# Kernel optimization log

Hardware: AMD Instinct MI355X
Metric: run time of the kernel (lower is better)

The kernel has to match this reference:

```python
import jax, jax.numpy as jnp
from jax import lax
import numpy as np

B, T, H, L = 4096, 7, 512, 256
D = 2 * H  # bidirectional LSTM feature dim


def _lstm(x, wih, whh, bih, bhh, reverse):
    # x: [B, T, L]; torch gate order i, f, g, o
    b, hdim = x.shape[0], whh.shape[0]
    xs = jnp.swapaxes(x, 0, 1)  # [T, B, L]
    bias = bih + bhh

    def step(carry, xt):
        h, c = carry
        gates = xt @ wih + h @ whh + bias
        i, f, g, o = jnp.split(gates, 4, axis=-1)
        c = jax.nn.sigmoid(f) * c + jax.nn.sigmoid(i) * jnp.tanh(g)
        h = jax.nn.sigmoid(o) * jnp.tanh(c)
        return (h, c), h

    h0 = jnp.zeros((b, hdim), x.dtype)
    _, hs = lax.scan(step, (h0, h0), xs, reverse=reverse)
    return jnp.swapaxes(hs, 0, 1)  # [B, T, H]


def _att(enc, dec):
    # Sequential attention: keys/values start as enc and grow with each decoder output.
    keys = enc  # [B, T, D]
    outs = []
    for i in range(dec.shape[1]):  # fixed small T=7, Python loop is static
        q = dec[:, i, :]                                  # [B, D]
        scores = jnp.einsum('bd,btd->bt', q, keys)        # dot over features
        a = jax.nn.softmax(scores, axis=1)
        ctx = jnp.einsum('bt,btd->bd', a, keys)
        out = ctx + q
        outs.append(out)
        keys = jnp.concatenate([keys, out[:, None, :]], axis=1)
    return jnp.stack(outs, axis=1)  # [B, T, D]


def _deconv(x, w, b):
    # torch ConvTranspose2d (stride 1, pad 0) == full conv with flipped, in/out-swapped kernel
    kh, kw = w.shape[2], w.shape[3]
    w2 = jnp.transpose(w[:, :, ::-1, ::-1], (1, 0, 2, 3))  # [out, in, kh, kw]
    y = lax.conv_general_dilated(x, w2, (1, 1), ((kh - 1, kh - 1), (kw - 1, kw - 1)),
                                 dimension_numbers=('NCHW', 'OIHW', 'NCHW'))
    return y + b[None, :, None, None]


def setup_inputs() -> dict:
    key = jax.random.key(0)
    ks = jax.random.split(key, 12)
    p = lambda k, shape: jax.random.normal(k, shape, jnp.float32) * 0.02
    return {
        'lstm_enc': jax.random.normal(ks[0], (B, T, D), jnp.float32),
        'gaussian_noise': jax.random.normal(ks[1], (B, L), jnp.float32),
        'embedrep_w': p(ks[2], (L, L * T)), 'embedrep_b': jnp.zeros((L * T,), jnp.float32),
        'wih_f': p(ks[3], (L, 4 * H)), 'whh_f': p(ks[4], (H, 4 * H)),
        'bih_f': jnp.zeros((4 * H,), jnp.float32), 'bhh_f': jnp.zeros((4 * H,), jnp.float32),
        'wih_b': p(ks[5], (L, 4 * H)), 'whh_b': p(ks[6], (H, 4 * H)),
        'bih_b': jnp.zeros((4 * H,), jnp.float32), 'bhh_b': jnp.zeros((4 * H,), jnp.float32),
        'emb_w': p(ks[7], (D, 1024)), 'emb_b': jnp.zeros((1024,), jnp.float32),
        'dc3_w': p(ks[8], (64, 32, 1, 3)), 'dc3_b': jnp.zeros((32,), jnp.float32),
        'dc1_w': p(ks[9], (32, 16, 1, 5)), 'dc1_b': jnp.zeros((16,), jnp.float32),
        'dc2_w': p(ks[10], (16, 1, 3, 3)), 'dc2_b': jnp.zeros((1,), jnp.float32),
        'infer': 0,
    }


def reference(lstm_enc, gaussian_noise, embedrep_w, embedrep_b,
              wih_f, whh_f, bih_f, bhh_f, wih_b, whh_b, bih_b, bhh_b,
              emb_w, emb_b, dc3_w, dc3_b, dc1_w, dc1_b, dc2_w, dc2_b, infer):
    b = lstm_enc.shape[0]
    g1 = jax.nn.soft_sign(gaussian_noise @ embedrep_w + embedrep_b)   # [B, L*T]
    rep = g1.reshape(b, T, L)                                          # [B, 7, L]
    hf = _lstm(rep, wih_f, whh_f, bih_f, bhh_f, False)
    hb = _lstm(rep, wih_b, whh_b, bih_b, bhh_b, True)
    lstm1 = jnp.concatenate([hf, hb], axis=-1)                         # [B, 7, 2H]
    att_out = _att(lstm_enc, lstm1)                                    # [B, 7, 2H]
    emb = att_out @ emb_w + emb_b                                      # [B, 7, 1024]
    up = jax.nn.soft_sign(emb).reshape(b * T, 64, 1, 16)
    x = jax.nn.leaky_relu(_deconv(up, dc3_w, dc3_b))                   # [B*7, 32, 1, 18]
    x = jax.nn.leaky_relu(_deconv(x, dc1_w, dc1_b))                    # [B*7, 16, 1, 22]
    x = jax.nn.leaky_relu(_deconv(x, dc2_w, dc2_b))                    # [B*7, 1, 3, 24]
    x = jax.nn.softmax(x, axis=2)                                      # softmax over H dim (=3)
    out = x.reshape(b, T, 1, 3, 24)[:, :, -1, :, :]                    # [B, 7, 3, 24]
    return out
```

## Files before the change

### kernel.cpp

```cpp
#include <hip/hip_runtime.h>
#include <stdint.h>


typedef __attribute__((ext_vector_type(4))) float f32x4;
typedef __attribute__((ext_vector_type(8))) short bf16x8;
typedef __attribute__((ext_vector_type(4))) unsigned short us4;

__device__ __forceinline__ unsigned short f2b(float f) {
  union { float f; unsigned u; } x; x.f = f;
  unsigned r = x.u + 0x7FFFu + ((x.u >> 16) & 1u);
  return (unsigned short)(r >> 16);
}
__device__ __forceinline__ float b2f(unsigned short s) {
  union { unsigned u; float f; } x; x.u = ((unsigned)s) << 16; return x.f;
}
__device__ __forceinline__ float sigmoidf(float x) {
  return 1.f / (1.f + __expf(-x));
}
__device__ __forceinline__ float fast_tanh(float x) {
  x = fminf(15.f, fmaxf(-15.f, x));
  float e = __expf(2.f * x);
  return (e - 1.f) / (e + 1.f);
}

__device__ __forceinline__ void gl_lds16(const void* g, void* l) {
  auto gp = reinterpret_cast<const __attribute__((address_space(1))) unsigned int*>(
      reinterpret_cast<uintptr_t>(g));
  auto lp = reinterpret_cast<__attribute__((address_space(3))) unsigned int*>(
      reinterpret_cast<uintptr_t>(l));
  __builtin_amdgcn_global_load_lds(gp, lp, 16, 0, 0);
}


__device__ __forceinline__ void stage256x32(const unsigned short* src, int ld,
                                            unsigned short* hbase, int tid) {
  const int row_in = tid >> 2;
  const int gidx = tid & 3;
#pragma unroll
  for (int r = 0; r < 4; ++r) {
    int row = r * 64 + row_in;
    int gsrc = gidx ^ ((row >> 1) & 3);
    gl_lds16(src + (size_t)row * ld + gsrc * 8, hbase + r * 2048 + (tid >> 6) * 512);
  }
}

__device__ __forceinline__ void stage128x32(const unsigned short* src, int ld,
                                            unsigned short* hbase, int tid) {
  const int row_in = tid >> 2;
  const int gidx = tid & 3;
#pragma unroll
  for (int r = 0; r < 2; ++r) {
    int row = r * 64 + row_in;
    int gsrc = gidx ^ ((row >> 1) & 3);
    gl_lds16(src + (size_t)row * ld + gsrc * 8, hbase + r * 2048 + (tid >> 6) * 512);
  }
}

__device__ __forceinline__ bf16x8 lds_fragH(const unsigned short* hbase, int row, int lq) {
  return *(const bf16x8*)(hbase + row * 32 + (lq ^ (((row >> 1) & 3) << 3)));
}

__device__ __forceinline__ void tile_w128(const unsigned short* Ab, const unsigned short* Bb,
                                          int wm, int wn, int lane, f32x4 (&acc)[8][4]) {
  const int lr = lane & 15, lq = (lane >> 4) * 8;
  bf16x8 b[4];
#pragma unroll
  for (int n = 0; n < 4; ++n) b[n] = lds_fragH(Bb, wn * 64 + n * 16 + lr, lq);
  bf16x8 a[8];
#pragma unroll
  for (int i = 0; i < 8; ++i) a[i] = lds_fragH(Ab, wm * 128 + i * 16 + lr, lq);
  __builtin_amdgcn_s_setprio(1);
#pragma unroll
  for (int i = 0; i < 8; ++i)
#pragma unroll
    for (int n = 0; n < 4; ++n)
      acc[i][n] = __builtin_amdgcn_mfma_f32_16x16x32_bf16(a[i], b[n], acc[i][n], 0, 0, 0);
  __builtin_amdgcn_s_setprio(0);
}

#define DBUF_SYNC()                                   \
  asm volatile("s_waitcnt vmcnt(0)" ::: "memory");    \
  __builtin_amdgcn_s_barrier();                       \
  __builtin_amdgcn_sched_barrier(0);

__device__ __forceinline__ void stage128x64(const unsigned short* src, int ld,
                                            unsigned short* lds, int wv, int lane) {
#pragma unroll
  for (int r = 0; r < 4; ++r) {
    int row = r * 32 + wv * 8 + (lane >> 3);
    gl_lds16(src + (size_t)row * ld + (lane & 7) * 8, lds + (r * 32 + wv * 8) * 64);
  }
}
__device__ __forceinline__ void mfma_tile(const unsigned short* As, const unsigned short* Bs,
                                          int wm, int wn, int lane, f32x4 acc[4][4]) {
#pragma unroll
  for (int kk = 0; kk < 2; ++kk) {
    int ko = kk * 32 + (lane >> 4) * 8;
    bf16x8 a[4], b[4];
#pragma unroll
    for (int i = 0; i < 4; ++i)
      a[i] = *(const bf16x8*)(As + (size_t)(wm * 64 + i * 16 + (lane & 15)) * 64 + ko);
#pragma unroll
    for (int i = 0; i < 4; ++i)
      b[i] = *(const bf16x8*)(Bs + (size_t)(wn * 64 + i * 16 + (lane & 15)) * 64 + ko);
#pragma unroll
    for (int mi = 0; mi < 4; ++mi)
#pragma unroll
      for (int ni = 0; ni < 4; ++ni)
        acc[mi][ni] = __builtin_amdgcn_mfma_f32_16x16x32_bf16(a[mi], b[ni], acc[mi][ni], 0, 0, 0);
  }
}

__global__ __launch_bounds__(256) void pack_kernel(
    const float* __restrict__ noise, const float* __restrict__ erep_w,
    const float* __restrict__ emb_w,
    const float* __restrict__ wih_f, const float* __restrict__ whh_f,
    const float* __restrict__ bih_f, const float* __restrict__ bhh_f,
    const float* __restrict__ wih_b, const float* __restrict__ whh_b,
    const float* __restrict__ bih_b, const float* __restrict__ bhh_b,
    unsigned short* __restrict__ noiseb, unsigned short* __restrict__ erepT,
    unsigned short* __restrict__ embT, unsigned short* __restrict__ lstmW,
    float* __restrict__ lstmB) {
  const int N0 = 4096 * 256;
  const int N1 = 1792 * 256;
  const int N2 = 1024 * 1024;
  const int N3 = 2 * 2048 * 768;
  const int N4 = 2 * 2048;
  const int total = N0 + N1 + N2 + N3 + N4;
  for (int i = blockIdx.x * 256 + threadIdx.x; i < total; i += gridDim.x * 256) {
    int x = i;
    if (x < N0) { noiseb[x] = f2b(noise[x]); continue; }
    x -= N0;
    if (x < N1) { int n = x >> 8, k = x & 255; erepT[x] = f2b(erep_w[k * 1792 + n]); continue; }
    x -= N1;
    if (x < N2) {
      int n = x >> 10, k = x & 1023;
      int o = (n & 63) * 16 + (n >> 6);
      embT[x] = f2b(emb_w[k * 1024 + o]);
      continue;
    }
    x -= N2;
    if (x < N3) {
      int dir = x / (2048 * 768);
      int r = x - dir * (2048 * 768);
      int npk = r / 768, k = r - (r / 768) * 768;
      int blk = npk >> 6, g = (npk >> 4) & 3, u = npk & 15;
      int o = g * 512 + blk * 16 + u;
      const float* wih = dir ? wih_b : wih_f;
      const float* whh = dir ? whh_b : whh_f;
      float v = (k < 256) ? wih[k * 2048 + o] : whh[(k - 256) * 2048 + o];
      lstmW[x] = f2b(v);
      continue;
    }
    x -= N3;
    {
      int dir = x >> 11, npk = x & 2047;
      int blk = npk >> 6, g = (npk >> 4) & 3, u = npk & 15;
      int o = g * 512 + blk * 16 + u;
      lstmB[x] = dir ? (bih_b[o] + bhh_b[o]) : (bih_f[o] + bhh_f[o]);
    }
  }
}

__global__ __launch_bounds__(256) void gemm_rep_kernel(
    const unsigned short* __restrict__ A, const unsigned short* __restrict__ Bt,
    const float* __restrict__ bias, unsigned short* __restrict__ rep_t) {
  __shared__ unsigned short As[128 * 64];
  __shared__ unsigned short Bs[128 * 64];
  const int lane = threadIdx.x & 63, wv = threadIdx.x >> 6;
  const int wm = wv >> 1, wn = wv & 1;
  const int m0 = blockIdx.y * 128, n0 = blockIdx.x * 128;
  f32x4 acc[4][4];
#pragma unroll
  for (int i = 0; i < 4; ++i)
#pragma unroll
    for (int j = 0; j < 4; ++j) acc[i][j] = (f32x4){0.f, 0.f, 0.f, 0.f};
  for (int k0 = 0; k0 < 256; k0 += 64) {
    stage128x64(A + (size_t)m0 * 256 + k0, 256, As, wv, lane);
    stage128x64(Bt + (size_t)n0 * 256 + k0, 256, Bs, wv, lane);
    __syncthreads();
    mfma_tile(As, Bs, wm, wn, lane, acc);
    __syncthreads();
  }
#pragma unroll
  for (int ni = 0; ni < 4; ++ni) {
    int n = n0 + wn * 64 + ni * 16 + (lane & 15);
    float bv = bias[n];
    int t = n >> 8, l = n & 255;
#pragma unroll
    for (int mi = 0; mi < 4; ++mi)
#pragma unroll
      for (int r = 0; r < 4; ++r) {
        int m = m0 + wm * 64 + mi * 16 + (lane >> 4) * 4 + r;
        float v = acc[mi][ni][r] + bv;
        v = v / (1.f + fabsf(v));
        rep_t[((size_t)t * 4096 + m) * 256 + l] = f2b(v);
      }
  }
}

__global__ __launch_bounds__(256, 2) void lstm_step_kernel(
    const unsigned short* __restrict__ rep_t, const unsigned short* __restrict__ Wp,
    const float* __restrict__ biasP, unsigned short* __restrict__ hbuf,
    unsigned short* __restrict__ cbuf, unsigned short* __restrict__ lstm1, int step) {
  __shared__ unsigned short Ar[2][8192];
  __shared__ unsigned short Br[2][4096];
  const int tid = threadIdx.x, lane = tid & 63, wv = tid >> 6;
  const int wm = wv >> 1, wn = wv & 1;
  const int swz = (blockIdx.x & 7) * 64 + (blockIdx.x >> 3);
  const int dir = swz >> 8;
  const int rem = swz & 255;
  const int by = rem >> 4, bx = rem & 15;
  const int m0 = by * 256, n0 = bx * 128;
  const int t_proc = dir ? (6 - step) : step;
  const unsigned short* W = Wp + (size_t)dir * 2048 * 768;
  const unsigned short* hin = hbuf + ((size_t)(step & 1) * 2 + dir) * (4096 * 512);
  unsigned short* hout = hbuf + ((size_t)((step + 1) & 1) * 2 + dir) * (4096 * 512);
  unsigned short* cp = cbuf + (size_t)dir * (4096 * 512);
  const unsigned short* xsrc = rep_t + (size_t)t_proc * 4096 * 256;

  f32x4 acc[8][4];
#pragma unroll
  for (int i = 0; i < 8; ++i)
#pragma unroll
    for (int j = 0; j < 4; ++j) acc[i][j] = (f32x4){0.f, 0.f, 0.f, 0.f};

  auto asrc = [&](int tt) {
    return tt < 8 ? xsrc + (size_t)m0 * 256 + tt * 32
                  : hin + (size_t)m0 * 512 + (tt - 8) * 32;
  };
  auto ald = [&](int tt) { return tt < 8 ? 256 : 512; };

  stage256x32(asrc(0), ald(0), Ar[0], tid);
  stage128x32(W + (size_t)n0 * 768 + 0 * 32, 768, Br[0], tid);
  DBUF_SYNC()

#pragma unroll
  for (int t = 0; t < 24; ++t) {
    if (t + 1 < 24) {
      stage256x32(asrc(t + 1), ald(t + 1), Ar[(t + 1) & 1], tid);
      stage128x32(W + (size_t)n0 * 768 + (t + 1) * 32, 768, Br[(t + 1) & 1], tid);
    }
    tile_w128(Ar[t & 1], Br[t & 1], wm, wn, lane, acc);
    if (t + 1 < 24) { DBUF_SYNC() }
  }

  const int u = lane & 15;
  const int blk = (n0 + wn * 64) >> 6;
  const int j = blk * 16 + u;
  const float bz0 = biasP[dir * 2048 + blk * 64 + 0 * 16 + u];
  const float bz1 = biasP[dir * 2048 + blk * 64 + 1 * 16 + u];
  const float bz2 = biasP[dir * 2048 + blk * 64 + 2 * 16 + u];
  const float bz3 = biasP[dir * 2048 + blk * 64 + 3 * 16 + u];
#pragma unroll
  for (int mi = 0; mi < 8; ++mi)
#pragma unroll
    for (int r = 0; r < 4; ++r) {
      int row = m0 + wm * 128 + mi * 16 + (lane >> 4) * 4 + r;
      float gi = acc[mi][0][r] + bz0;
      float gf = acc[mi][1][r] + bz1;
      float gg = acc[mi][2][r] + bz2;
      float go = acc[mi][3][r] + bz3;
      size_t ci = (size_t)row * 512 + j;
      float c = sigmoidf(gf) * b2f(cp[ci]) + sigmoidf(gi) * fast_tanh(gg);
      cp[ci] = f2b(c);
      float h = sigmoidf(go) * fast_tanh(c);
      unsigned short hb = f2b(h);
      hout[ci] = hb;
      lstm1[((size_t)row * 7 + t_proc) * 1024 + dir * 512 + j] = hb;
    }
}

__global__ __launch_bounds__(256) void att_fused3_kernel(
    const float* __restrict__ enc, const unsigned short* __restrict__ lstm1,
    unsigned short* __restrict__ att) {
  __shared__ unsigned short Qs[7 * 1032];
  __shared__ unsigned short Es[7 * 1032];
  __shared__ float P[8 * 256];
  __shared__ float sG[98];
  __shared__ float sC[7][14];
  __shared__ float sA[16];
  const int tid = threadIdx.x, lane = tid & 63, wv = tid >> 6;
  const int b = blockIdx.x;
  const float* Eb = enc + (size_t)b * 7168;
  const unsigned short* Qb = lstm1 + (size_t)b * 7168;

  if (tid < 98) ((float*)sC)[tid] = 0.f;

  const f32x4* Eb4 = (const f32x4*)Eb;
  const int d0 = tid * 4;
#pragma unroll
  for (int r = 0; r < 7; ++r) {
    f32x4 v = Eb4[r * 256 + tid];
    us4 hi;
#pragma unroll
    for (int e = 0; e < 4; ++e) hi[e] = f2b(v[e]);
    *(us4*)&Es[r * 1032 + d0] = hi;
    *(us4*)&Qs[r * 1032 + d0] = *(const us4*)(Qb + r * 1024 + d0);
  }
  asm volatile("s_waitcnt lgkmcnt(0)" ::: "memory");
  __builtin_amdgcn_sched_barrier(0);

  {
    const int rr = lane & 15;
    const int rowc = rr % 7;
    const int kbase = wv * 256 + (lane >> 4) * 8;
    f32x4 g1 = {0.f, 0.f, 0.f, 0.f}, g2 = {0.f, 0.f, 0.f, 0.f};
#pragma unroll
    for (int s = 0; s < 8; ++s) {
      const int k0 = kbase + s * 32;
      bf16x8 aq = *(const bf16x8*)&Qs[rowc * 1032 + k0];
      bf16x8 be = *(const bf16x8*)&Es[rowc * 1032 + k0];
      g1 = __builtin_amdgcn_mfma_f32_16x16x32_bf16(aq, be, g1, 0, 0, 0);
      g2 = __builtin_amdgcn_mfma_f32_16x16x32_bf16(aq, aq, g2, 0, 0, 0);
    }
    *(f32x4*)&P[((wv * 2 + 0) * 64 + lane) * 4] = g1;
    *(f32x4*)&P[((wv * 2 + 1) * 64 + lane) * 4] = g2;
  }
  __syncthreads();

  if (tid < 98) {
    int i = tid / 14, v = tid - i * 14;
    int col = v < 7 ? v : v - 7;
    int tile = v < 7 ? 0 : 1;
    int ln = ((i >> 2) << 4) | col;
    int rg = i & 3;
    float s = 0.f;
#pragma unroll
    for (int w = 0; w < 4; ++w) s += P[((w * 2 + tile) * 64 + ln) * 4 + rg];
    sG[i * 14 + v] = s;
  }
  __syncthreads();
  if (wv == 0) {
    for (int i = 0; i < 7; ++i) {
      const int nt = 7 + i;
      float s = -1e30f;
      if (lane < 7) {
        s = sG[i * 14 + lane];
      } else if (lane < nt) {
        int jj = lane - 7;
        float a2 = 0.f;
#pragma unroll
        for (int v = 0; v < 14; ++v) a2 += sC[jj][v] * sG[i * 14 + v];
        s = a2;
      }
      float mx = s;
#pragma unroll
      for (int off = 8; off >= 1; off >>= 1) mx = fmaxf(mx, __shfl_xor(mx, off, 16));
      float e = (lane < nt) ? __expf(s - mx) : 0.f;
      float sum = e;
#pragma unroll
      for (int off = 8; off >= 1; off >>= 1) sum += __shfl_xor(sum, off, 16);
      float aw = e / sum;
      if (lane < 16) sA[lane] = aw;
      if (lane < 14) {
        float c = (lane < 7) ? sA[lane] : 0.f;
        for (int jj = 0; jj < i; ++jj) c += sA[7 + jj] * sC[jj][lane];
        if (lane == 7 + i) c += 1.f;
        sC[i][lane] = c;
      }
    }
  }
  __syncthreads();

  {
    float acc[7][4];
#pragma unroll
    for (int i = 0; i < 7; ++i)
#pragma unroll
      for (int e = 0; e < 4; ++e) acc[i][e] = 0.f;
#pragma unroll
    for (int t = 0; t < 7; ++t) {
      us4 ev = *(const us4*)&Es[t * 1032 + d0];
      float evf[4];
#pragma unroll
      for (int e = 0; e < 4; ++e) evf[e] = b2f(ev[e]);
#pragma unroll
      for (int i = 0; i < 7; ++i) {
        float c = sC[i][t];
#pragma unroll
        for (int e = 0; e < 4; ++e) acc[i][e] += c * evf[e];
      }
    }
#pragma unroll
    for (int m = 0; m < 7; ++m) {
      us4 qv = *(const us4*)&Qs[m * 1032 + d0];
      float qf[4];
#pragma unroll
      for (int e = 0; e < 4; ++e) qf[e] = b2f(qv[e]);
#pragma unroll
      for (int i = m; i < 7; ++i) {
        float c = sC[i][7 + m];
#pragma unroll
        for (int e = 0; e < 4; ++e) acc[i][e] += c * qf[e];
      }
    }
    unsigned short* Ab = att + (size_t)b * 7168;
#pragma unroll
    for (int i = 0; i < 7; ++i) {
      us4 r;
#pragma unroll
      for (int e = 0; e < 4; ++e) r[e] = f2b(acc[i][e]);
      *(us4*)(Ab + i * 1024 + d0) = r;
    }
  }
}

__global__ __launch_bounds__(256, 2) void gemm_emb_kernel(
    const unsigned short* __restrict__ A, const unsigned short* __restrict__ Bt,
    const float* __restrict__ bias, unsigned short* __restrict__ up_t) {
  __shared__ unsigned short Ar[2][8192];
  __shared__ unsigned short Br[2][4096];
  const int tid = threadIdx.x, lane = tid & 63, wv = tid >> 6;
  const int wm = wv >> 1, wn = wv & 1;
  const int swz = (blockIdx.x & 7) * 112 + (blockIdx.x >> 3);
  const int by = swz >> 3, bx = swz & 7;
  const int m0 = by * 256, n0 = bx * 128;

  f32x4 acc[8][4];
#pragma unroll
  for (int i = 0; i < 8; ++i)
#pragma unroll
    for (int j = 0; j < 4; ++j) acc[i][j] = (f32x4){0.f, 0.f, 0.f, 0.f};

  const unsigned short* Abase = A + (size_t)m0 * 1024;
  const unsigned short* Bbase = Bt + (size_t)n0 * 1024;

  stage256x32(Abase + 0 * 32, 1024, Ar[0], tid);
  stage128x32(Bbase + 0 * 32, 1024, Br[0], tid);
  DBUF_SYNC()

#pragma unroll
  for (int t = 0; t < 32; ++t) {
    if (t + 1 < 32) {
      stage256x32(Abase + (t + 1) * 32, 1024, Ar[(t + 1) & 1], tid);
      stage128x32(Bbase + (t + 1) * 32, 1024, Br[(t + 1) & 1], tid);
    }
    tile_w128(Ar[t & 1], Br[t & 1], wm, wn, lane, acc);
    if (t + 1 < 32) { DBUF_SYNC() }
  }

#pragma unroll
  for (int ni = 0; ni < 4; ++ni) {
    int np = n0 + wn * 64 + ni * 16 + (lane & 15);
    int o = (np & 63) * 16 + (np >> 6);
    float bv = bias[o];
#pragma unroll
    for (int mi = 0; mi < 8; ++mi)
#pragma unroll
      for (int r = 0; r < 4; ++r) {
        int m = m0 + wm * 128 + mi * 16 + (lane >> 4) * 4 + r;
        float v = acc[mi][ni][r] + bv;
        v = v / (1.f + fabsf(v));
        up_t[(size_t)m * 1024 + np] = f2b(v);
      }
  }
}

__global__ __launch_bounds__(256) void dc_fused_kernel(
    const unsigned short* __restrict__ up_t,
    const float* __restrict__ w3, const float* __restrict__ b3,
    const float* __restrict__ w1, const float* __restrict__ b1,
    const float* __restrict__ w2, const float* __restrict__ b2,
    float* __restrict__ out) {
  __shared__ unsigned short y1L[576 * 40];
  __shared__ unsigned short y2L[704 * 24];
  const int tid = threadIdx.x, lane = tid & 63, wv = tid >> 6;
  const int g0 = blockIdx.x * 32;
  const int kq = (lane >> 4) * 8;
  const int oc = lane & 15;

  {
    bf16x8 bf[2][6];
#pragma unroll
    for (int nt = 0; nt < 2; ++nt)
#pragma unroll
      for (int kk = 0; kk < 6; ++kk) {
        bf16x8 v;
#pragma unroll
        for (int t = 0; t < 8; ++t) {
          int k = kk * 32 + kq + t;
          int jj = k >> 6, ic = k & 63;
          v[t] = (short)f2b(w3[((size_t)ic * 32 + nt * 16 + oc) * 3 + jj]);
        }
        bf[nt][kk] = v;
      }
    const float bia0 = b3[oc], bia1 = b3[16 + oc];
    for (int c = wv; c < 36; c += 4) {
      int m = c * 16 + (lane & 15);
      int imgl = m / 18, ow = m - imgl * 18;
      const unsigned short* arow = up_t + (size_t)(g0 + imgl) * 1024;
      f32x4 acc0 = {0.f, 0.f, 0.f, 0.f}, acc1 = {0.f, 0.f, 0.f, 0.f};
#pragma unroll
      for (int kk = 0; kk < 6; ++kk) {
        int jj = kk >> 1;
        int ic0 = (kk & 1) * 32 + kq;
        int iw = ow - jj;
        bf16x8 a = {0, 0, 0, 0, 0, 0, 0, 0};
        if ((unsigned)iw < 16u) a = *(const bf16x8*)(arow + iw * 64 + ic0);
        acc0 = __builtin_amdgcn_mfma_f32_16x16x32_bf16(a, bf[0][kk], acc0, 0, 0, 0);
        acc1 = __builtin_amdgcn_mfma_f32_16x16x32_bf16(a, bf[1][kk], acc1, 0, 0, 0);
      }
#pragma unroll
      for (int r = 0; r < 4; ++r) {
        int mm = c * 16 + (lane >> 4) * 4 + r;
        float v0 = acc0[r] + bia0; v0 = v0 > 0.f ? v0 : 0.01f * v0;
        float v1 = acc1[r] + bia1; v1 = v1 > 0.f ? v1 : 0.01f * v1;
        y1L[mm * 40 + oc] = f2b(v0);
        y1L[mm * 40 + 16 + oc] = f2b(v1);
      }
    }
  }
  __syncthreads();

  {
    bf16x8 bf[5];
#pragma unroll
    for (int kk = 0; kk < 5; ++kk) {
      bf16x8 v;
#pragma unroll
      for (int t = 0; t < 8; ++t) {
        int ic = kq + t;
        v[t] = (short)f2b(w1[((size_t)ic * 16 + oc) * 5 + kk]);
      }
      bf[kk] = v;
    }
    const float bia = b1[oc];
    for (int c = wv; c < 44; c += 4) {
      int m = c * 16 + (lane & 15);
      int imgl = m / 22, ow = m - imgl * 22;
      const unsigned short* abase = y1L + imgl * (18 * 40);
      f32x4 acc = {0.f, 0.f, 0.f, 0.f};
#pragma unroll
      for (int kk = 0; kk < 5; ++kk) {
        int iw = ow - kk;
        bf16x8 a = {0, 0, 0, 0, 0, 0, 0, 0};
        if ((unsigned)iw < 18u) a = *(const bf16x8*)(abase + iw * 40 + kq);
        acc = __builtin_amdgcn_mfma_f32_16x16x32_bf16(a, bf[kk], acc, 0, 0, 0);
      }
#pragma unroll
      for (int r = 0; r < 4; ++r) {
        int mm = c * 16 + (lane >> 4) * 4 + r;
        float v = acc[r] + bia;
        v = v > 0.f ? v : 0.01f * v;
        y2L[mm * 24 + oc] = f2b(v);
      }
    }
  }
  __syncthreads();

  for (int ii = tid; ii < 768; ii += 256) {
    int imgl = ii / 24, ow = ii - imgl * 24;
    float lg0 = b2[0], lg1 = b2[0], lg2 = b2[0];
#pragma unroll
    for (int jj = 0; jj < 3; ++jj) {
      int iw = ow - jj;
      if ((unsigned)iw >= 22u) continue;
      const unsigned short* row = y2L + (imgl * 22 + iw) * 24;
      bf16x8 v0 = *(const bf16x8*)(row);
      bf16x8 v1 = *(const bf16x8*)(row + 8);
      float x[16];
#pragma unroll
      for (int ic = 0; ic < 8; ++ic) {
        x[ic] = b2f((unsigned short)v0[ic]);
        x[8 + ic] = b2f((unsigned short)v1[ic]);
      }
#pragma unroll
      for (int ic = 0; ic < 16; ++ic) {
        lg0 += x[ic] * w2[ic * 9 + 0 * 3 + jj];
        lg1 += x[ic] * w2[ic * 9 + 1 * 3 + jj];
        lg2 += x[ic] * w2[ic * 9 + 2 * 3 + jj];
      }
    }
    lg0 = lg0 > 0.f ? lg0 : 0.01f * lg0;
    lg1 = lg1 > 0.f ? lg1 : 0.01f * lg1;
    lg2 = lg2 > 0.f ? lg2 : 0.01f * lg2;
    float mx = fmaxf(lg0, fmaxf(lg1, lg2));
    float e0 = __expf(lg0 - mx), e1 = __expf(lg1 - mx), e2 = __expf(lg2 - mx);
    float inv = 1.f / (e0 + e1 + e2);
    size_t ob = (size_t)(g0 + imgl) * 72 + ow;
    out[ob] = e0 * inv;
    out[ob + 24] = e1 * inv;
    out[ob + 48] = e2 * inv;
  }
}

extern "C" void kernel_launch(void* const* d_in, const int* in_sizes, int n_in,
                              void* d_out, int out_size, void* d_ws, size_t ws_size,
                              hipStream_t stream) {
  (void)in_sizes; (void)n_in; (void)out_size; (void)ws_size;
  const float* enc    = (const float*)d_in[0];
  const float* noise  = (const float*)d_in[1];
  const float* erep_w = (const float*)d_in[2];
  const float* erep_b = (const float*)d_in[3];
  const float* wih_f  = (const float*)d_in[4];
  const float* whh_f  = (const float*)d_in[5];
  const float* bih_f  = (const float*)d_in[6];
  const float* bhh_f  = (const float*)d_in[7];
  const float* wih_b  = (const float*)d_in[8];
  const float* whh_b  = (const float*)d_in[9];
  const float* bih_b  = (const float*)d_in[10];
  const float* bhh_b  = (const float*)d_in[11];
  const float* emb_w  = (const float*)d_in[12];
  const float* emb_b  = (const float*)d_in[13];
  const float* dc3w   = (const float*)d_in[14];
  const float* dc3b   = (const float*)d_in[15];
  const float* dc1w   = (const float*)d_in[16];
  const float* dc1b   = (const float*)d_in[17];
  const float* dc2w   = (const float*)d_in[18];
  const float* dc2b   = (const float*)d_in[19];
  float* out = (float*)d_out;

  char* p = (char*)d_ws;
  auto carve = [&p](size_t bytes) {
    char* r = p;
    p += (bytes + 255) & ~(size_t)255;
    return r;
  };
  unsigned short* rep_t  = (unsigned short*)carve(7ull * 4096 * 256 * 2);
  unsigned short* lstmW  = (unsigned short*)carve(2ull * 2048 * 768 * 2);
  float*          lstmB  = (float*)carve(2ull * 2048 * 4);
  unsigned short* noiseb = (unsigned short*)carve(4096ull * 256 * 2);
  unsigned short* erepT  = (unsigned short*)carve(1792ull * 256 * 2);
  unsigned short* embT   = (unsigned short*)carve(1024ull * 1024 * 2);
  unsigned short* hbuf   = (unsigned short*)carve(4ull * 4096 * 512 * 2);
  unsigned short* cbuf   = (unsigned short*)carve(2ull * 4096 * 512 * 2);
  unsigned short* lstm1  = (unsigned short*)carve(4096ull * 7 * 1024 * 2);
  unsigned short* att    = (unsigned short*)carve(28672ull * 1024 * 2);
  unsigned short* up_t   = (unsigned short*)carve(28672ull * 1024 * 2);

  hipMemsetAsync(hbuf, 0, 2ull * 4096 * 512 * 2, stream);
  hipMemsetAsync(cbuf, 0, 2ull * 4096 * 512 * 2, stream);

  pack_kernel<<<2048, 256, 0, stream>>>(noise, erep_w, emb_w, wih_f, whh_f, bih_f, bhh_f,
                                        wih_b, whh_b, bih_b, bhh_b,
                                        noiseb, erepT, embT, lstmW, lstmB);
  gemm_rep_kernel<<<dim3(14, 32), 256, 0, stream>>>(noiseb, erepT, erep_b, rep_t);
  for (int s = 0; s < 7; ++s)
    lstm_step_kernel<<<512, 256, 0, stream>>>(rep_t, lstmW, lstmB, hbuf, cbuf, lstm1, s);
  att_fused3_kernel<<<4096, 256, 0, stream>>>(enc, lstm1, att);
  gemm_emb_kernel<<<896, 256, 0, stream>>>(att, embT, emb_b, up_t);
  dc_fused_kernel<<<896, 256, 0, stream>>>(up_t, dc3w, dc3b, dc1w, dc1b, dc2w, dc2b, out);
}
```

Measured before the change: 497.1 us.

## Halve LSTM step tile to 128 rows with 2-wave blocks; vectorize pack kernel

Each LSTM step block now covers a 128x128 output tile with 128 threads (2 waves), and twice as many blocks are launched. The goal is more blocks per step so the GPU's CUs are better filled. Separately, the weight-pack kernel now converts four elements per thread and writes them as one vector store. The smaller tile gives up some reuse of the weight tile across rows and adds more staging traffic per output.

```diff
diff --git a/kernel.cpp b/kernel.cpp
--- a/kernel.cpp
+++ b/kernel.cpp
@@ -53,6 +53,18 @@
     int row = r * 64 + row_in;
     int gsrc = gidx ^ ((row >> 1) & 3);
     gl_lds16(src + (size_t)row * ld + gsrc * 8, hbase + r * 2048 + (tid >> 6) * 512);
+  }
+}
+
+__device__ __forceinline__ void stage128x32_t128(const unsigned short* src, int ld,
+                                                 unsigned short* hbase, int tid) {
+  const int row_in = tid >> 2;
+  const int gidx = tid & 3;
+#pragma unroll
+  for (int r = 0; r < 4; ++r) {
+    int row = r * 32 + row_in;
+    int gsrc = gidx ^ ((row >> 1) & 3);
+    gl_lds16(src + (size_t)row * ld + gsrc * 8, hbase + r * 1024 + (tid >> 6) * 512);
   }
 }
 
@@ -121,43 +133,71 @@
     unsigned short* __restrict__ noiseb, unsigned short* __restrict__ erepT,
     unsigned short* __restrict__ embT, unsigned short* __restrict__ lstmW,
     float* __restrict__ lstmB) {
-  const int N0 = 4096 * 256;
-  const int N1 = 1792 * 256;
-  const int N2 = 1024 * 1024;
-  const int N3 = 2 * 2048 * 768;
-  const int N4 = 2 * 2048;
+  const int N0 = 4096 * 256 / 4;
+  const int N1 = 1792 * 256 / 4;
+  const int N2 = 1024 * 1024 / 4;
+  const int N3 = 2 * 2048 * 768 / 4;
+  const int N4 = 2 * 2048 / 4;
   const int total = N0 + N1 + N2 + N3 + N4;
   for (int i = blockIdx.x * 256 + threadIdx.x; i < total; i += gridDim.x * 256) {
     int x = i;
-    if (x < N0) { noiseb[x] = f2b(noise[x]); continue; }
+    if (x < N0) {
+      f32x4 v = ((const f32x4*)noise)[x];
+      us4 o4;
+#pragma unroll
+      for (int e = 0; e < 4; ++e) o4[e] = f2b(v[e]);
+      ((us4*)noiseb)[x] = o4;
+      continue;
+    }
     x -= N0;
-    if (x < N1) { int n = x >> 8, k = x & 255; erepT[x] = f2b(erep_w[k * 1792 + n]); continue; }
+    if (x < N1) {
+      int n = x >> 6, k4 = (x & 63) * 4;
+      us4 o4;
+#pragma unroll
+      for (int e = 0; e < 4; ++e) o4[e] = f2b(erep_w[(size_t)(k4 + e) * 1792 + n]);
+      ((us4*)erepT)[x] = o4;
+      continue;
+    }
     x -= N1;
     if (x < N2) {
-      int n = x >> 10, k = x & 1023;
+      int n = x >> 8, k4 = (x & 255) * 4;
       int o = (n & 63) * 16 + (n >> 6);
-      embT[x] = f2b(emb_w[k * 1024 + o]);
+      us4 o4;
+#pragma unroll
+      for (int e = 0; e < 4; ++e) o4[e] = f2b(emb_w[(size_t)(k4 + e) * 1024 + o]);
+      ((us4*)embT)[x] = o4;
       continue;
     }
     x -= N2;
     if (x < N3) {
-      int dir = x / (2048 * 768);
-      int r = x - dir * (2048 * 768);
-      int npk = r / 768, k = r - (r / 768) * 768;
+      int dir = x / (2048 * 192);
+      int r = x - dir * (2048 * 192);
+      int npk = r / 192, k4 = (r - npk * 192) * 4;
       int blk = npk >> 6, g = (npk >> 4) & 3, u = npk & 15;
       int o = g * 512 + blk * 16 + u;
       const float* wih = dir ? wih_b : wih_f;
       const float* whh = dir ? whh_b : whh_f;
-      float v = (k < 256) ? wih[k * 2048 + o] : whh[(k - 256) * 2048 + o];
-      lstmW[x] = f2b(v);
+      us4 o4;
+#pragma unroll
+      for (int e = 0; e < 4; ++e) {
+        int k = k4 + e;
+        float v = (k < 256) ? wih[(size_t)k * 2048 + o] : whh[(size_t)(k - 256) * 2048 + o];
+        o4[e] = f2b(v);
+      }
+      ((us4*)lstmW)[x] = o4;
       continue;
     }
     x -= N3;
     {
-      int dir = x >> 11, npk = x & 2047;
-      int blk = npk >> 6, g = (npk >> 4) & 3, u = npk & 15;
+      int dir = x >> 9, npk4 = (x & 511) * 4;
+      int blk = npk4 >> 6, g = (npk4 >> 4) & 3, u = npk4 & 15;
       int o = g * 512 + blk * 16 + u;
-      lstmB[x] = dir ? (bih_b[o] + bhh_b[o]) : (bih_f[o] + bhh_f[o]);
+      const float* bi = dir ? bih_b : bih_f;
+      const float* bh = dir ? bhh_b : bhh_f;
+      f32x4 o4;
+#pragma unroll
+      for (int e = 0; e < 4; ++e) o4[e] = bi[o + e] + bh[o + e];
+      ((f32x4*)lstmB)[x] = o4;
     }
   }
 }
@@ -199,19 +239,18 @@
   }
 }
 
-__global__ __launch_bounds__(256, 2) void lstm_step_kernel(
+__global__ __launch_bounds__(128, 2) void lstm_step_kernel(
     const unsigned short* __restrict__ rep_t, const unsigned short* __restrict__ Wp,
     const float* __restrict__ biasP, unsigned short* __restrict__ hbuf,
     unsigned short* __restrict__ cbuf, unsigned short* __restrict__ lstm1, int step) {
-  __shared__ unsigned short Ar[2][8192];
+  __shared__ unsigned short Ar[2][4096];
   __shared__ unsigned short Br[2][4096];
   const int tid = threadIdx.x, lane = tid & 63, wv = tid >> 6;
-  const int wm = wv >> 1, wn = wv & 1;
-  const int swz = (blockIdx.x & 7) * 64 + (blockIdx.x >> 3);
-  const int dir = swz >> 8;
-  const int rem = swz & 255;
+  const int swz = (blockIdx.x & 7) * 128 + (blockIdx.x >> 3);
+  const int dir = swz >> 9;
+  const int rem = swz & 511;
   const int by = rem >> 4, bx = rem & 15;
-  const int m0 = by * 256, n0 = bx * 128;
+  const int m0 = by * 128, n0 = bx * 128;
   const int t_proc = dir ? (6 - step) : step;
   const unsigned short* W = Wp + (size_t)dir * 2048 * 768;
   const unsigned short* hin = hbuf + ((size_t)(step & 1) * 2 + dir) * (4096 * 512);
@@ -231,22 +270,22 @@
   };
   auto ald = [&](int tt) { return tt < 8 ? 256 : 512; };
 
-  stage256x32(asrc(0), ald(0), Ar[0], tid);
-  stage128x32(W + (size_t)n0 * 768 + 0 * 32, 768, Br[0], tid);
+  stage128x32_t128(asrc(0), ald(0), Ar[0], tid);
+  stage128x32_t128(W + (size_t)n0 * 768 + 0 * 32, 768, Br[0], tid);
   DBUF_SYNC()
 
 #pragma unroll
   for (int t = 0; t < 24; ++t) {
     if (t + 1 < 24) {
-      stage256x32(asrc(t + 1), ald(t + 1), Ar[(t + 1) & 1], tid);
-      stage128x32(W + (size_t)n0 * 768 + (t + 1) * 32, 768, Br[(t + 1) & 1], tid);
-    }
-    tile_w128(Ar[t & 1], Br[t & 1], wm, wn, lane, acc);
+      stage128x32_t128(asrc(t + 1), ald(t + 1), Ar[(t + 1) & 1], tid);
+      stage128x32_t128(W + (size_t)n0 * 768 + (t + 1) * 32, 768, Br[(t + 1) & 1], tid);
+    }
+    tile_w128(Ar[t & 1], Br[t & 1], 0, wv, lane, acc);
     if (t + 1 < 24) { DBUF_SYNC() }
   }
 
   const int u = lane & 15;
-  const int blk = (n0 + wn * 64) >> 6;
+  const int blk = (n0 + wv * 64) >> 6;
   const int j = blk * 16 + u;
   const float bz0 = biasP[dir * 2048 + blk * 64 + 0 * 16 + u];
   const float bz1 = biasP[dir * 2048 + blk * 64 + 1 * 16 + u];
@@ -256,7 +295,7 @@
   for (int mi = 0; mi < 8; ++mi)
 #pragma unroll
     for (int r = 0; r < 4; ++r) {
-      int row = m0 + wm * 128 + mi * 16 + (lane >> 4) * 4 + r;
+      int row = m0 + mi * 16 + (lane >> 4) * 4 + r;
       float gi = acc[mi][0][r] + bz0;
       float gf = acc[mi][1][r] + bz1;
       float gg = acc[mi][2][r] + bz2;
@@ -637,7 +676,7 @@
                                         noiseb, erepT, embT, lstmW, lstmB);
   gemm_rep_kernel<<<dim3(14, 32), 256, 0, stream>>>(noiseb, erepT, erep_b, rep_t);
   for (int s = 0; s < 7; ++s)
-    lstm_step_kernel<<<512, 256, 0, stream>>>(rep_t, lstmW, lstmB, hbuf, cbuf, lstm1, s);
+    lstm_step_kernel<<<1024, 128, 0, stream>>>(rep_t, lstmW, lstmB, hbuf, cbuf, lstm1, s);
   att_fused3_kernel<<<4096, 256, 0, stream>>>(enc, lstm1, att);
   gemm_emb_kernel<<<896, 256, 0, stream>>>(att, embT, emb_b, up_t);
   dc_fused_kernel<<<896, 256, 0, stream>>>(up_t, dc3w, dc3b, dc1w, dc1b, dc2w, dc2b, out);
```

Measured after the change: 523.2 us. 1.05x slower.
